# Optimization experiments

Hardware: AMD Instinct MI355X
Metric: run time of the kernel (lower is better)

The kernel has to match this reference:

```python
import jax, jax.numpy as jnp
import numpy as np


def setup_inputs() -> dict:
    key = jax.random.key(0)
    ks = jax.random.split(key, 8)
    B, C, H, W = 4, 256, 64, 64
    Cqk = C // 8
    s = 0.05
    return {
        "x": jax.random.normal(ks[0], (B, C, H, W), jnp.float32),
        "Wq": jax.random.normal(ks[1], (Cqk, C), jnp.float32) * s,
        "bq": jax.random.normal(ks[2], (Cqk,), jnp.float32) * s,
        "Wk": jax.random.normal(ks[3], (Cqk, C), jnp.float32) * s,
        "bk": jax.random.normal(ks[4], (Cqk,), jnp.float32) * s,
        "Wv": jax.random.normal(ks[5], (C, C), jnp.float32) * s,
        "bv": jax.random.normal(ks[6], (C,), jnp.float32) * s,
        "gamma": jax.random.normal(ks[7], (1,), jnp.float32),
    }


def reference(x, Wq, bq, Wk, bk, Wv, bv, gamma):
    B, C, H, W = x.shape
    N = H * W
    xf = x.reshape(B, C, N)                      # [B,C,N]
    # 1x1 convs == channel matmuls
    q = jnp.einsum('oc,bcn->bon', Wq, xf) + bq[None, :, None]   # [B,C/8,N]
    k = jnp.einsum('oc,bcn->bon', Wk, xf) + bk[None, :, None]   # [B,C/8,N]
    v = jnp.einsum('oc,bcn->bon', Wv, xf) + bv[None, :, None]   # [B,C,N]
    # scores[b,i,j] = <q[:,i], k[:,j]>; softmax over j (last dim)
    scores = jnp.einsum('bci,bcj->bij', q, k)                   # [B,N,N]
    attn = jax.nn.softmax(scores, axis=-1)
    # out[b,c,i] = sum_j v[b,c,j] * attn[b,i,j]
    out = jnp.einsum('bcj,bij->bci', v, attn).reshape(B, C, H, W)
    return gamma[0] * out + x
```

## Files before the change

kernel.cpp:

```cpp
#include <hip/hip_runtime.h>


#define B_ 4
#define C_ 256
#define N_ 4096
#define CQK 32

typedef __attribute__((ext_vector_type(8))) short short8;
typedef __attribute__((ext_vector_type(4))) short short4v;
typedef __attribute__((ext_vector_type(16))) float f32x16;
typedef __attribute__((ext_vector_type(4))) float f32x4;

__device__ __forceinline__ unsigned short f2bf(float f) {
  unsigned int u = __builtin_bit_cast(unsigned int, f);
  u = (u + 0x7fffu + ((u >> 16) & 1u)) >> 16;
  return (unsigned short)u;
}
__device__ __forceinline__ float bf2f(unsigned short s) {
  unsigned int u = ((unsigned int)s) << 16;
  return __builtin_bit_cast(float, u);
}
__device__ __forceinline__ f32x16 mfma16(short8 a, short8 b, f32x16 c) {
  return __builtin_amdgcn_mfma_f32_32x32x16_bf16(a, b, c, 0, 0, 0);
}
__device__ __forceinline__ int swz64(int row, int col) {
  return row * 64 + ((((col >> 3) ^ row) & 7) << 3) + (col & 7);
}
__device__ __forceinline__ int swz32(int row, int col) {
  return row * 32 + ((((col >> 3) ^ row) & 3) << 3) + (col & 7);
}

__global__ __launch_bounds__(256) void k_prep(
    const float* __restrict__ x, unsigned short* __restrict__ xthi,
    unsigned short* __restrict__ xtlo,
    const float* __restrict__ Wq, const float* __restrict__ Wk,
    const float* __restrict__ Wv,
    unsigned short* __restrict__ wqh, unsigned short* __restrict__ wql,
    unsigned short* __restrict__ wkh, unsigned short* __restrict__ wkl,
    unsigned short* __restrict__ wvh, unsigned short* __restrict__ wvl) {
  __shared__ __align__(16) float tile[64 * 65];
  const int bi = blockIdx.x;
  const int t = threadIdx.x;
  if (bi < 1024) {
    const int it = bi & 63, ct = (bi >> 6) & 3, b = bi >> 8;
    const int i0 = it * 64, c0 = ct * 64;
    {
      const int i = t & 63, cb = t >> 6;
#pragma unroll
      for (int z = 0; z < 16; ++z) {
        const int c = z * 4 + cb;
        tile[i * 65 + c] = x[(b * C_ + c0 + c) * N_ + i0 + i];
      }
    }
    __syncthreads();
    {
      const int ii = t >> 2, p = t & 3;
      short8 h0, h1, l0, l1;
#pragma unroll
      for (int e = 0; e < 16; ++e) {
        const float f = tile[ii * 65 + p * 16 + e];
        const unsigned short hb = f2bf(f);
        const unsigned short lb = f2bf(f - bf2f(hb));
        if (e < 8) { h0[e] = (short)hb; l0[e] = (short)lb; }
        else       { h1[e - 8] = (short)hb; l1[e - 8] = (short)lb; }
      }
      const int base = (b * N_ + i0 + ii) * C_ + c0 + p * 16;
      *(short8*)(xthi + base) = h0;
      *(short8*)(xthi + base + 8) = h1;
      *(short8*)(xtlo + base) = l0;
      *(short8*)(xtlo + base + 8) = l1;
    }
  } else {
    const int e = (bi - 1024) * 256 + t;
    const float* src; unsigned short *hi, *lo; int idx;
    if (e < 8192)        { src = Wq; hi = wqh; lo = wql; idx = e; }
    else if (e < 16384)  { src = Wk; hi = wkh; lo = wkl; idx = e - 8192; }
    else                 { src = Wv; hi = wvh; lo = wvl; idx = e - 16384; }
    const float f = src[idx];
    const unsigned short h = f2bf(f);
    hi[idx] = h;
    lo[idx] = f2bf(f - bf2f(h));
  }
}

__global__ __launch_bounds__(256) void k_proj(
    const unsigned short* __restrict__ wqh, const unsigned short* __restrict__ wql,
    const unsigned short* __restrict__ wkh, const unsigned short* __restrict__ wkl,
    const unsigned short* __restrict__ wvh, const unsigned short* __restrict__ wvl,
    const unsigned short* __restrict__ xthi, const unsigned short* __restrict__ xtlo,
    const float* __restrict__ bq, const float* __restrict__ bk,
    const float* __restrict__ bv,
    unsigned short* __restrict__ qhg, unsigned short* __restrict__ qlg,
    unsigned short* __restrict__ khg, unsigned short* __restrict__ klg,
    unsigned short* __restrict__ vg) {
  __shared__ __align__(16) char sm[33792];
  unsigned short* awh = (unsigned short*)sm;
  unsigned short* awl = awh + 4096;
  unsigned short* bxh = awl + 4096;
  unsigned short* bxl = bxh + 4096;
  float* qt = (float*)sm;

  const int it = blockIdx.x, ot = blockIdx.y, b = blockIdx.z;
  const int i0 = it * 64, o0 = ot * 64;
  const int t = threadIdx.x, lane = t & 63, w = t >> 6, h = lane >> 5;
  const int mb = w >> 1, nb = w & 1;
  const int srow = t >> 2, sp = t & 3;

  const int og = o0 + srow;
  const unsigned short *wh, *wl;
  if (og < 32)      { wh = wqh + og * C_;        wl = wql + og * C_; }
  else if (og < 64) { wh = wkh + (og - 32) * C_; wl = wkl + (og - 32) * C_; }
  else              { wh = wvh + (og - 64) * C_; wl = wvl + (og - 64) * C_; }
  const unsigned short* xh = xthi + (b * N_ + i0 + srow) * C_;
  const unsigned short* xl = xtlo + (b * N_ + i0 + srow) * C_;

  f32x16 acc;
#pragma unroll
  for (int e = 0; e < 16; ++e) acc[e] = 0.f;
  const int m = 32 * mb + (lane & 31);
  const int n = 32 * nb + (lane & 31);

  for (int kt = 0; kt < 4; ++kt) {
    const int cb = kt * 64 + sp * 16;
    *(short8*)&awh[swz64(srow, sp * 16)]     = *(const short8*)(wh + cb);
    *(short8*)&awh[swz64(srow, sp * 16 + 8)] = *(const short8*)(wh + cb + 8);
    *(short8*)&awl[swz64(srow, sp * 16)]     = *(const short8*)(wl + cb);
    *(short8*)&awl[swz64(srow, sp * 16 + 8)] = *(const short8*)(wl + cb + 8);
    *(short8*)&bxh[swz64(srow, sp * 16)]     = *(const short8*)(xh + cb);
    *(short8*)&bxh[swz64(srow, sp * 16 + 8)] = *(const short8*)(xh + cb + 8);
    *(short8*)&bxl[swz64(srow, sp * 16)]     = *(const short8*)(xl + cb);
    *(short8*)&bxl[swz64(srow, sp * 16 + 8)] = *(const short8*)(xl + cb + 8);
    __syncthreads();
#pragma unroll
    for (int kk = 0; kk < 4; ++kk) {
      const int kb = kk * 16 + h * 8;
      const short8 ah  = *(const short8*)&awh[swz64(m, kb)];
      const short8 al2 = *(const short8*)&awl[swz64(m, kb)];
      const short8 bh  = *(const short8*)&bxh[swz64(n, kb)];
      const short8 bl2 = *(const short8*)&bxl[swz64(n, kb)];
      acc = mfma16(ah, bh, acc);
      acc = mfma16(ah, bl2, acc);
      acc = mfma16(al2, bh, acc);
    }
    __syncthreads();
  }

  if (ot > 0) {
#pragma unroll
    for (int e = 0; e < 16; ++e) {
      const int r = 32 * mb + (e & 3) + 8 * (e >> 2) + 4 * h;
      const int oc = o0 - 64 + r;
      vg[(b * C_ + oc) * N_ + i0 + n] = f2bf(acc[e] + bv[oc]);
    }
  } else {
#pragma unroll
    for (int e = 0; e < 16; ++e) {
      const int r = 32 * mb + (e & 3) + 8 * (e >> 2) + 4 * h;
      const float bias = (r < 32) ? bq[r] : bk[r - 32];
      qt[r * 65 + n] = acc[e] + bias;
    }
    __syncthreads();
    const int ii = t >> 2;
    short8 hv0, hv1, lv0, lv1;
#pragma unroll
    for (int e = 0; e < 16; ++e) {
      const float f = qt[(sp * 16 + e) * 65 + ii];
      const unsigned short hb = f2bf(f);
      const unsigned short lb = f2bf(f - bf2f(hb));
      if (e < 8) { hv0[e] = (short)hb; lv0[e] = (short)lb; }
      else       { hv1[e - 8] = (short)hb; lv1[e - 8] = (short)lb; }
    }
    if (sp < 2) {
      const int base = (b * N_ + i0 + ii) * CQK + sp * 16;
      *(short8*)(qhg + base) = hv0; *(short8*)(qhg + base + 8) = hv1;
      *(short8*)(qlg + base) = lv0; *(short8*)(qlg + base + 8) = lv1;
    } else {
      const int base = (b * N_ + i0 + ii) * CQK + sp * 16 - 32;
      *(short8*)(khg + base) = hv0; *(short8*)(khg + base + 8) = hv1;
      *(short8*)(klg + base) = lv0; *(short8*)(klg + base + 8) = lv1;
    }
  }
}

__global__ __launch_bounds__(512, 4) void k_flash(
    const unsigned short* __restrict__ qhg, const unsigned short* __restrict__ qlg,
    const unsigned short* __restrict__ khg, const unsigned short* __restrict__ klg,
    const unsigned short* __restrict__ vg,
    unsigned short* __restrict__ Opart, float* __restrict__ mlpart) {
  __shared__ __align__(16) char sm[65536];
  unsigned short* kh = (unsigned short*)sm;
  unsigned short* kl = (unsigned short*)(sm + 4096);
  unsigned short* vt = (unsigned short*)(sm + 8192);
  float* stf = (float*)(sm + 40960);
  char* stb = sm + 40960;
  float* alphaf = (float*)(sm + 57344);
  float* otf = (float*)sm;

  const int blk = blockIdx.x;
  const int b = (blk >> 1) & 3;
  const int half = blk & 1;
  const int qt_ = blk >> 3;
  const int q0 = qt_ * 64;
  const int jbase = half * 2048;
  const int t = threadIdx.x, lane = t & 63, w = t >> 6, h = lane >> 5;
  const int l31 = lane & 31;
  const int r_sm = t >> 3, p_sm = t & 7;

  {
    const int r = (t & 255) >> 2, g = t & 3;
    const unsigned short* src = ((t < 256) ? qhg : qlg) + (b * N_ + q0 + r) * CQK + g * 8;
    unsigned short* dst = (t < 256) ? kh : kl;
    *(short8*)&dst[swz32(r, g * 8)] = *(const short8*)src;
  }
  __syncthreads();
  const int mbs = (w >> 1) & 1, nbs = w & 1;
  short8 qfh[2], qfl[2];
  {
    const int mq = 32 * mbs + l31;
#pragma unroll
    for (int kk = 0; kk < 2; ++kk) {
      qfh[kk] = *(const short8*)&kh[swz32(mq, kk * 16 + h * 8)];
      qfl[kk] = *(const short8*)&kl[swz32(mq, kk * 16 + h * 8)];
    }
  }
  __syncthreads();

  f32x16 acc0, acc1;
#pragma unroll
  for (int e = 0; e < 16; ++e) { acc0[e] = 0.f; acc1[e] = 0.f; }
  float m_run = -1e30f, l_run = 0.f;

  for (int kt = 0; kt < 32; ++kt) {
    const int j0 = jbase + kt * 64;
    {
      const int r = (t & 255) >> 2, g = t & 3;
      const unsigned short* src = ((t < 256) ? khg : klg) + (b * N_ + j0 + r) * CQK + g * 8;
      unsigned short* dst = (t < 256) ? kh : kl;
      *(short8*)&dst[swz32(r, g * 8)] = *(const short8*)src;
    }
#pragma unroll
    for (int pass = 0; pass < 4; ++pass) {
      const int gid = pass * 512 + t;
      const int c = gid >> 3, g = gid & 7;
      *(short8*)&vt[swz64(c, g * 8)] =
          *(const short8*)(vg + (b * C_ + c) * N_ + j0 + g * 8);
    }
    __syncthreads();
    if (w < 4) {
      f32x16 sa;
#pragma unroll
      for (int e = 0; e < 16; ++e) sa[e] = 0.f;
      const int jn = 32 * nbs + l31;
#pragma unroll
      for (int kk = 0; kk < 2; ++kk) {
        const short8 bh = *(const short8*)&kh[swz32(jn, kk * 16 + h * 8)];
        const short8 bl = *(const short8*)&kl[swz32(jn, kk * 16 + h * 8)];
        sa = mfma16(qfh[kk], bh, sa);
        sa = mfma16(qfh[kk], bl, sa);
        sa = mfma16(qfl[kk], bh, sa);
      }
#pragma unroll
      for (int e = 0; e < 16; ++e) {
        const int ri = 32 * mbs + (e & 3) + 8 * (e >> 2) + 4 * h;
        stf[ri * 64 + ((((jn >> 2) ^ ri) & 15) << 2) + (jn & 3)] = sa[e];
      }
    }
    __syncthreads();
    {
      float* p0 = stf + r_sm * 64 + ((((2 * p_sm) ^ r_sm) & 15) << 2);
      float* p1 = stf + r_sm * 64 + ((((2 * p_sm + 1) ^ r_sm) & 15) << 2);
      const f32x4 a0 = *(const f32x4*)p0;
      const f32x4 a1 = *(const f32x4*)p1;
      float s[8];
#pragma unroll
      for (int e = 0; e < 4; ++e) { s[e] = a0[e]; s[4 + e] = a1[e]; }
      float mx = s[0];
#pragma unroll
      for (int e = 1; e < 8; ++e) mx = fmaxf(mx, s[e]);
      mx = fmaxf(mx, __shfl_xor(mx, 1));
      mx = fmaxf(mx, __shfl_xor(mx, 2));
      mx = fmaxf(mx, __shfl_xor(mx, 4));
      const float mnew = fmaxf(m_run, mx);
      const float al = __expf(m_run - mnew);
      float ts = 0.f;
      short8 pv8;
#pragma unroll
      for (int e = 0; e < 8; ++e) {
        const float pe = __expf(s[e] - mnew);
        ts += pe;
        pv8[e] = (short)f2bf(pe);
      }
      ts += __shfl_xor(ts, 1);
      ts += __shfl_xor(ts, 2);
      ts += __shfl_xor(ts, 4);
      l_run = l_run * al + ts;
      m_run = mnew;
      *(short8*)p0 = pv8;
      if (p_sm == 0) alphaf[r_sm] = al;
    }
    __syncthreads();
#pragma unroll
    for (int eq = 0; eq < 4; ++eq) {
      const f32x4 av0 = *(const f32x4*)&alphaf[4 * h + 8 * eq];
      const f32x4 av1 = *(const f32x4*)&alphaf[32 + 4 * h + 8 * eq];
#pragma unroll
      for (int q = 0; q < 4; ++q) {
        acc0[4 * eq + q] *= av0[q];
        acc1[4 * eq + q] *= av1[q];
      }
    }
    {
      const int crow = 32 * w + l31;
#pragma unroll
      for (int kk = 0; kk < 4; ++kk) {
        const int g0 = ((4 * kk + 2 * h) ^ l31) & 15;
        const short8 pa0 = *(const short8*)(stb + l31 * 256 + (g0 << 4));
        const short8 pa1 = *(const short8*)(stb + (32 + l31) * 256 + (g0 << 4));
        const short8 vf = *(const short8*)&vt[swz64(crow, kk * 16 + h * 8)];
        acc0 = mfma16(pa0, vf, acc0);
        acc1 = mfma16(pa1, vf, acc1);
      }
    }
    __syncthreads();
  }

  if (p_sm == 0) {
    mlpart[blk * 128 + r_sm] = m_run;
    mlpart[blk * 128 + 64 + r_sm] = l_run;
  }
  {
    const int cc = 32 * w + l31;
#pragma unroll
    for (int e = 0; e < 16; ++e) {
      const int r0 = (e & 3) + 8 * (e >> 2) + 4 * h;
      otf[cc * 64 + ((((r0 >> 2) ^ cc) & 15) << 2) + (r0 & 3)] = acc0[e];
      const int r1 = 32 + r0;
      otf[cc * 64 + ((((r1 >> 2) ^ cc) & 15) << 2) + (r1 & 3)] = acc1[e];
    }
  }
  __syncthreads();
#pragma unroll
  for (int pass = 0; pass < 8; ++pass) {
    const int idx = pass * 512 + t;
    const int c = idx >> 4, gi = idx & 15;
    const f32x4 ov = *(const f32x4*)(otf + c * 64 + (((gi ^ c) & 15) << 2));
    short4v hv;
#pragma unroll
    for (int q = 0; q < 4; ++q) {
      const _Float16 hf = (_Float16)ov[q];
      hv[q] = __builtin_bit_cast(short, hf);
    }
    *(short4v*)(Opart + blk * 16384 + c * 64 + gi * 4) = hv;
  }
}

__global__ __launch_bounds__(256) void k_combine(
    const unsigned short* __restrict__ Opart, const float* __restrict__ mlpart,
    const float* __restrict__ x, const float* __restrict__ gamma,
    float* __restrict__ out) {
  const int cb = blockIdx.x;
  const int b = cb & 3, qt_ = cb >> 2;
  const int q0 = qt_ * 64;
  const int blk1 = (qt_ << 3) | (b << 1);
  const int blk2 = blk1 | 1;
  const int t = threadIdx.x;
  const int i = t & 63, cg = t >> 6;

  const float m1 = mlpart[blk1 * 128 + i], l1 = mlpart[blk1 * 128 + 64 + i];
  const float m2 = mlpart[blk2 * 128 + i], l2 = mlpart[blk2 * 128 + 64 + i];
  const float M = fmaxf(m1, m2);
  const float w1 = __expf(m1 - M), w2 = __expf(m2 - M);
  const float inv = 1.f / (w1 * l1 + w2 * l2);
  const float gm = gamma[0];
  const float s1 = gm * w1 * inv, s2 = gm * w2 * inv;

  const unsigned short* p1 = Opart + blk1 * 16384 + i;
  const unsigned short* p2 = Opart + blk2 * 16384 + i;
#pragma unroll 4
  for (int c = cg; c < C_; c += 4) {
    const float o1 = (float)__builtin_bit_cast(_Float16, p1[c * 64]);
    const float o2 = (float)__builtin_bit_cast(_Float16, p2[c * 64]);
    const int g = (b * C_ + c) * N_ + q0 + i;
    out[g] = s1 * o1 + s2 * o2 + x[g];
  }
}

extern "C" void kernel_launch(void* const* d_in, const int* in_sizes, int n_in,
                              void* d_out, int out_size, void* d_ws, size_t ws_size,
                              hipStream_t stream) {
  const float* x     = (const float*)d_in[0];
  const float* Wq    = (const float*)d_in[1];
  const float* bq    = (const float*)d_in[2];
  const float* Wk    = (const float*)d_in[3];
  const float* bk    = (const float*)d_in[4];
  const float* Wv    = (const float*)d_in[5];
  const float* bv    = (const float*)d_in[6];
  const float* gamma = (const float*)d_in[7];
  float* out = (float*)d_out;
  (void)in_sizes; (void)n_in; (void)out_size; (void)ws_size;

  char* ws = (char*)d_ws;
  size_t off = 0;
  auto carve = [&](size_t bytes) -> char* {
    char* p = ws + off;
    off += (bytes + 255) & ~(size_t)255;
    return p;
  };
  unsigned short* xthi = (unsigned short*)carve((size_t)B_ * N_ * C_ * 2);
  unsigned short* xtlo = (unsigned short*)carve((size_t)B_ * N_ * C_ * 2);
  unsigned short* wqh  = (unsigned short*)carve(32 * 256 * 2);
  unsigned short* wql  = (unsigned short*)carve(32 * 256 * 2);
  unsigned short* wkh  = (unsigned short*)carve(32 * 256 * 2);
  unsigned short* wkl  = (unsigned short*)carve(32 * 256 * 2);
  unsigned short* wvh  = (unsigned short*)carve(256 * 256 * 2);
  unsigned short* wvl  = (unsigned short*)carve(256 * 256 * 2);
  unsigned short* qhg  = (unsigned short*)carve((size_t)B_ * N_ * CQK * 2);
  unsigned short* qlg  = (unsigned short*)carve((size_t)B_ * N_ * CQK * 2);
  unsigned short* khg  = (unsigned short*)carve((size_t)B_ * N_ * CQK * 2);
  unsigned short* klg  = (unsigned short*)carve((size_t)B_ * N_ * CQK * 2);
  unsigned short* vg   = (unsigned short*)carve((size_t)B_ * C_ * N_ * 2);
  unsigned short* Opart = (unsigned short*)carve((size_t)512 * 16384 * 2);
  float* mlpart = (float*)carve((size_t)512 * 128 * 4);

  k_prep<<<1344, 256, 0, stream>>>(x, xthi, xtlo, Wq, Wk, Wv,
                                   wqh, wql, wkh, wkl, wvh, wvl);
  k_proj<<<dim3(64, 5, B_), 256, 0, stream>>>(wqh, wql, wkh, wkl, wvh, wvl,
                                              xthi, xtlo, bq, bk, bv,
                                              qhg, qlg, khg, klg, vg);
  k_flash<<<512, 512, 0, stream>>>(qhg, qlg, khg, klg, vg, Opart, mlpart);
  k_combine<<<256, 256, 0, stream>>>(Opart, mlpart, x, gamma, out);
}
```

Before: 213.9 us.

## Prefetch K and V through registers, drop K LDS staging and barriers

K fragments for the QK^T MFMAs now load straight from global into registers, one tile ahead, so K is no longer staged in shared memory. The next V tile is register-prefetched two tiles ahead and written only to the LDS rows owned by the same wave, which removes a full block barrier per iteration. Some barriers become raw s_barrier with explicit lgkmcnt waits, and setprio raises wave priority around the MFMA sections. The trade-off is higher register pressure and reliance on per-wave ownership of V rows for correctness without a sync.

```diff
diff --git a/kernel.cpp b/kernel.cpp
--- a/kernel.cpp
+++ b/kernel.cpp
@@ -26,9 +26,13 @@
 __device__ __forceinline__ int swz64(int row, int col) {
   return row * 64 + ((((col >> 3) ^ row) & 7) << 3) + (col & 7);
 }
-__device__ __forceinline__ int swz32(int row, int col) {
-  return row * 32 + ((((col >> 3) ^ row) & 3) << 3) + (col & 7);
-}
+
+#define BAR_SYNC                                        \
+  do {                                                  \
+    asm volatile("s_waitcnt lgkmcnt(0)" ::: "memory");  \
+    __builtin_amdgcn_s_barrier();                       \
+  } while (0)
+#define BAR_FAST __builtin_amdgcn_s_barrier()
 
 __global__ __launch_bounds__(256) void k_prep(
     const float* __restrict__ x, unsigned short* __restrict__ xthi,
@@ -188,12 +192,10 @@
     const unsigned short* __restrict__ vg,
     unsigned short* __restrict__ Opart, float* __restrict__ mlpart) {
   __shared__ __align__(16) char sm[65536];
-  unsigned short* kh = (unsigned short*)sm;
-  unsigned short* kl = (unsigned short*)(sm + 4096);
-  unsigned short* vt = (unsigned short*)(sm + 8192);
-  float* stf = (float*)(sm + 40960);
-  char* stb = sm + 40960;
-  float* alphaf = (float*)(sm + 57344);
+  float* stf = (float*)sm;
+  char* stb = sm;
+  unsigned short* vt = (unsigned short*)(sm + 16384);
+  float* alphaf = (float*)(sm + 49152);
   float* otf = (float*)sm;
 
   const int blk = blockIdx.x;
@@ -205,25 +207,42 @@
   const int t = threadIdx.x, lane = t & 63, w = t >> 6, h = lane >> 5;
   const int l31 = lane & 31;
   const int r_sm = t >> 3, p_sm = t & 7;
-
-  {
-    const int r = (t & 255) >> 2, g = t & 3;
-    const unsigned short* src = ((t < 256) ? qhg : qlg) + (b * N_ + q0 + r) * CQK + g * 8;
-    unsigned short* dst = (t < 256) ? kh : kl;
-    *(short8*)&dst[swz32(r, g * 8)] = *(const short8*)src;
-  }
-  __syncthreads();
   const int mbs = (w >> 1) & 1, nbs = w & 1;
-  short8 qfh[2], qfl[2];
-  {
-    const int mq = 32 * mbs + l31;
+
+  const int vrow = 32 * w + (lane >> 3);
+  const int vcol = (lane & 7) * 8;
+  const unsigned short* vsrc =
+      vg + (size_t)(b * C_ + vrow) * N_ + jbase + vcol;
+
+  short8 vst[4];
+#pragma unroll
+  for (int p = 0; p < 4; ++p)
+    vst[p] = *(const short8*)(vsrc + p * 8 * N_);
+
+  short8 qfh[2], qfl[2], kfh[2], kfl[2];
+  const unsigned short* qph =
+      qhg + (size_t)(b * N_ + q0 + 32 * mbs + l31) * CQK + h * 8;
+  const unsigned short* qpl =
+      qlg + (size_t)(b * N_ + q0 + 32 * mbs + l31) * CQK + h * 8;
+  const unsigned short* kph =
+      khg + (size_t)(b * N_ + jbase + 32 * nbs + l31) * CQK + h * 8;
+  const unsigned short* kpl =
+      klg + (size_t)(b * N_ + jbase + 32 * nbs + l31) * CQK + h * 8;
+  if (w < 4) {
 #pragma unroll
     for (int kk = 0; kk < 2; ++kk) {
-      qfh[kk] = *(const short8*)&kh[swz32(mq, kk * 16 + h * 8)];
-      qfl[kk] = *(const short8*)&kl[swz32(mq, kk * 16 + h * 8)];
-    }
-  }
-  __syncthreads();
+      qfh[kk] = *(const short8*)(qph + kk * 16);
+      qfl[kk] = *(const short8*)(qpl + kk * 16);
+      kfh[kk] = *(const short8*)(kph + kk * 16);
+      kfl[kk] = *(const short8*)(kpl + kk * 16);
+    }
+  }
+#pragma unroll
+  for (int p = 0; p < 4; ++p)
+    *(short8*)&vt[swz64(vrow + 8 * p, vcol)] = vst[p];
+#pragma unroll
+  for (int p = 0; p < 4; ++p)
+    vst[p] = *(const short8*)(vsrc + 64 + p * 8 * N_);
 
   f32x16 acc0, acc1;
 #pragma unroll
@@ -231,41 +250,33 @@
   float m_run = -1e30f, l_run = 0.f;
 
   for (int kt = 0; kt < 32; ++kt) {
-    const int j0 = jbase + kt * 64;
-    {
-      const int r = (t & 255) >> 2, g = t & 3;
-      const unsigned short* src = ((t < 256) ? khg : klg) + (b * N_ + j0 + r) * CQK + g * 8;
-      unsigned short* dst = (t < 256) ? kh : kl;
-      *(short8*)&dst[swz32(r, g * 8)] = *(const short8*)src;
-    }
-#pragma unroll
-    for (int pass = 0; pass < 4; ++pass) {
-      const int gid = pass * 512 + t;
-      const int c = gid >> 3, g = gid & 7;
-      *(short8*)&vt[swz64(c, g * 8)] =
-          *(const short8*)(vg + (b * C_ + c) * N_ + j0 + g * 8);
-    }
-    __syncthreads();
+    BAR_FAST;
     if (w < 4) {
       f32x16 sa;
 #pragma unroll
       for (int e = 0; e < 16; ++e) sa[e] = 0.f;
+      __builtin_amdgcn_s_setprio(1);
+#pragma unroll
+      for (int kk = 0; kk < 2; ++kk) {
+        sa = mfma16(qfh[kk], kfh[kk], sa);
+        sa = mfma16(qfh[kk], kfl[kk], sa);
+        sa = mfma16(qfl[kk], kfh[kk], sa);
+      }
+      __builtin_amdgcn_s_setprio(0);
       const int jn = 32 * nbs + l31;
-#pragma unroll
-      for (int kk = 0; kk < 2; ++kk) {
-        const short8 bh = *(const short8*)&kh[swz32(jn, kk * 16 + h * 8)];
-        const short8 bl = *(const short8*)&kl[swz32(jn, kk * 16 + h * 8)];
-        sa = mfma16(qfh[kk], bh, sa);
-        sa = mfma16(qfh[kk], bl, sa);
-        sa = mfma16(qfl[kk], bh, sa);
-      }
 #pragma unroll
       for (int e = 0; e < 16; ++e) {
         const int ri = 32 * mbs + (e & 3) + 8 * (e >> 2) + 4 * h;
         stf[ri * 64 + ((((jn >> 2) ^ ri) & 15) << 2) + (jn & 3)] = sa[e];
       }
-    }
-    __syncthreads();
+      const int ko = ((kt + 1 < 32) ? (kt + 1) : 31) * 64 * CQK;
+#pragma unroll
+      for (int kk = 0; kk < 2; ++kk) {
+        kfh[kk] = *(const short8*)(kph + ko + kk * 16);
+        kfl[kk] = *(const short8*)(kpl + ko + kk * 16);
+      }
+    }
+    BAR_SYNC;
     {
       float* p0 = stf + r_sm * 64 + ((((2 * p_sm) ^ r_sm) & 15) << 2);
       float* p1 = stf + r_sm * 64 + ((((2 * p_sm + 1) ^ r_sm) & 15) << 2);
@@ -298,7 +309,7 @@
       *(short8*)p0 = pv8;
       if (p_sm == 0) alphaf[r_sm] = al;
     }
-    __syncthreads();
+    BAR_SYNC;
 #pragma unroll
     for (int eq = 0; eq < 4; ++eq) {
       const f32x4 av0 = *(const f32x4*)&alphaf[4 * h + 8 * eq];
@@ -311,6 +322,7 @@
     }
     {
       const int crow = 32 * w + l31;
+      __builtin_amdgcn_s_setprio(1);
 #pragma unroll
       for (int kk = 0; kk < 4; ++kk) {
         const int g0 = ((4 * kk + 2 * h) ^ l31) & 15;
@@ -320,14 +332,22 @@
         acc0 = mfma16(pa0, vf, acc0);
         acc1 = mfma16(pa1, vf, acc1);
       }
-    }
-    __syncthreads();
+      __builtin_amdgcn_s_setprio(0);
+    }
+#pragma unroll
+    for (int p = 0; p < 4; ++p)
+      *(short8*)&vt[swz64(vrow + 8 * p, vcol)] = vst[p];
+    const int vo = ((kt + 2 < 32) ? (kt + 2) : 31) * 64;
+#pragma unroll
+    for (int p = 0; p < 4; ++p)
+      vst[p] = *(const short8*)(vsrc + vo + p * 8 * N_);
   }
 
   if (p_sm == 0) {
     mlpart[blk * 128 + r_sm] = m_run;
     mlpart[blk * 128 + 64 + r_sm] = l_run;
   }
+  BAR_FAST;
   {
     const int cc = 32 * w + l31;
 #pragma unroll
@@ -338,7 +358,7 @@
       otf[cc * 64 + ((((r1 >> 2) ^ cc) & 15) << 2) + (r1 & 3)] = acc1[e];
     }
   }
-  __syncthreads();
+  BAR_SYNC;
 #pragma unroll
   for (int pass = 0; pass < 8; ++pass) {
     const int idx = pass * 512 + t;
```

Result: slower. 243.6 us (+13.9%).

## Prefetch K/V tiles via direct global-to-LDS loads overlapped with compute

Applied to the files above, without the earlier changes.

Replaces the per-iteration register-staged K and V tile loads in the flash kernel with global_load_lds async copies. The next K tile is issued after the score stage and the next V tile after the PV MFMAs, and they are synchronised with explicit s_waitcnt vmcnt counters and raw barriers instead of __syncthreads. The Q fragments are now loaded straight from global memory into registers, the LDS regions are rearranged so the score buffer no longer overlaps K/V, and s_setprio is raised around the MFMA blocks. The goal is to hide global latency behind compute. The cost is fragile manual counter-based synchronisation, and there is a risk of races if the vmcnt accounting is wrong.

```diff
diff --git a/kernel.cpp b/kernel.cpp
--- a/kernel.cpp
+++ b/kernel.cpp
@@ -29,6 +29,18 @@
 __device__ __forceinline__ int swz32(int row, int col) {
   return row * 32 + ((((col >> 3) ^ row) & 3) << 3) + (col & 7);
 }
+
+#define GL16(gp, lp)                                                     \
+  __builtin_amdgcn_global_load_lds(                                      \
+      (const __attribute__((address_space(1))) unsigned int*)(gp),       \
+      (__attribute__((address_space(3))) unsigned int*)(lp), 16, 0, 0)
+
+#define WAITCNT(s) asm volatile("s_waitcnt " s ::: "memory")
+#define BARRIER()                         \
+  do {                                    \
+    __builtin_amdgcn_s_barrier();         \
+    asm volatile("" ::: "memory");        \
+  } while (0)
 
 __global__ __launch_bounds__(256) void k_prep(
     const float* __restrict__ x, unsigned short* __restrict__ xthi,
@@ -188,11 +200,11 @@
     const unsigned short* __restrict__ vg,
     unsigned short* __restrict__ Opart, float* __restrict__ mlpart) {
   __shared__ __align__(16) char sm[65536];
-  unsigned short* kh = (unsigned short*)sm;
-  unsigned short* kl = (unsigned short*)(sm + 4096);
-  unsigned short* vt = (unsigned short*)(sm + 8192);
-  float* stf = (float*)(sm + 40960);
-  char* stb = sm + 40960;
+  float* stf = (float*)sm;
+  char* stb = sm;
+  unsigned short* kh = (unsigned short*)(sm + 16384);
+  unsigned short* kl = (unsigned short*)(sm + 20480);
+  unsigned short* vt = (unsigned short*)(sm + 24576);
   float* alphaf = (float*)(sm + 57344);
   float* otf = (float*)sm;
 
@@ -205,25 +217,38 @@
   const int t = threadIdx.x, lane = t & 63, w = t >> 6, h = lane >> 5;
   const int l31 = lane & 31;
   const int r_sm = t >> 3, p_sm = t & 7;
-
-  {
-    const int r = (t & 255) >> 2, g = t & 3;
-    const unsigned short* src = ((t < 256) ? qhg : qlg) + (b * N_ + q0 + r) * CQK + g * 8;
-    unsigned short* dst = (t < 256) ? kh : kl;
-    *(short8*)&dst[swz32(r, g * 8)] = *(const short8*)src;
-  }
-  __syncthreads();
   const int mbs = (w >> 1) & 1, nbs = w & 1;
+
+  const int krow = 16 * (w & 3) + (lane >> 2);
+  const int kg = (lane & 3) ^ (krow & 3);
+  const unsigned short* kgsrc = ((w < 4) ? khg : klg) +
+      (size_t)(b * N_ + jbase + krow) * CQK + kg * 8;
+  unsigned short* kldst = ((w < 4) ? kh : kl) + (w & 3) * 512;
+  const int vc = 32 * w + (lane >> 3);
+  const int vgg = (lane & 7) ^ ((lane >> 3) & 7);
+  const unsigned short* vgsrc =
+      vg + (size_t)(b * C_ + vc) * N_ + jbase + vgg * 8;
+  unsigned short* vldst = vt + 32 * w * 64;
+
+  GL16(kgsrc, kldst);
+#pragma unroll
+  for (int q = 0; q < 4; ++q)
+    GL16(vgsrc + q * 8 * N_, vldst + q * 8 * 64);
+
   short8 qfh[2], qfl[2];
   {
-    const int mq = 32 * mbs + l31;
-#pragma unroll
-    for (int kk = 0; kk < 2; ++kk) {
-      qfh[kk] = *(const short8*)&kh[swz32(mq, kk * 16 + h * 8)];
-      qfl[kk] = *(const short8*)&kl[swz32(mq, kk * 16 + h * 8)];
-    }
-  }
-  __syncthreads();
+    const unsigned short* qph =
+        qhg + (size_t)(b * N_ + q0 + 32 * mbs + l31) * CQK + h * 8;
+    const unsigned short* qpl =
+        qlg + (size_t)(b * N_ + q0 + 32 * mbs + l31) * CQK + h * 8;
+    if (w < 4) {
+#pragma unroll
+      for (int kk = 0; kk < 2; ++kk) {
+        qfh[kk] = *(const short8*)(qph + kk * 16);
+        qfl[kk] = *(const short8*)(qpl + kk * 16);
+      }
+    }
+  }
 
   f32x16 acc0, acc1;
 #pragma unroll
@@ -231,26 +256,14 @@
   float m_run = -1e30f, l_run = 0.f;
 
   for (int kt = 0; kt < 32; ++kt) {
-    const int j0 = jbase + kt * 64;
-    {
-      const int r = (t & 255) >> 2, g = t & 3;
-      const unsigned short* src = ((t < 256) ? khg : klg) + (b * N_ + j0 + r) * CQK + g * 8;
-      unsigned short* dst = (t < 256) ? kh : kl;
-      *(short8*)&dst[swz32(r, g * 8)] = *(const short8*)src;
-    }
-#pragma unroll
-    for (int pass = 0; pass < 4; ++pass) {
-      const int gid = pass * 512 + t;
-      const int c = gid >> 3, g = gid & 7;
-      *(short8*)&vt[swz64(c, g * 8)] =
-          *(const short8*)(vg + (b * C_ + c) * N_ + j0 + g * 8);
-    }
-    __syncthreads();
+    WAITCNT("vmcnt(4) lgkmcnt(0)");
+    BARRIER();
     if (w < 4) {
       f32x16 sa;
 #pragma unroll
       for (int e = 0; e < 16; ++e) sa[e] = 0.f;
       const int jn = 32 * nbs + l31;
+      __builtin_amdgcn_s_setprio(1);
 #pragma unroll
       for (int kk = 0; kk < 2; ++kk) {
         const short8 bh = *(const short8*)&kh[swz32(jn, kk * 16 + h * 8)];
@@ -259,13 +272,19 @@
         sa = mfma16(qfh[kk], bl, sa);
         sa = mfma16(qfl[kk], bh, sa);
       }
+      __builtin_amdgcn_s_setprio(0);
 #pragma unroll
       for (int e = 0; e < 16; ++e) {
         const int ri = 32 * mbs + (e & 3) + 8 * (e >> 2) + 4 * h;
         stf[ri * 64 + ((((jn >> 2) ^ ri) & 15) << 2) + (jn & 3)] = sa[e];
       }
     }
-    __syncthreads();
+    WAITCNT("lgkmcnt(0)");
+    BARRIER();
+    {
+      const int ktn = (kt + 1 < 32) ? kt + 1 : 31;
+      GL16(kgsrc + ktn * 64 * CQK, kldst);
+    }
     {
       float* p0 = stf + r_sm * 64 + ((((2 * p_sm) ^ r_sm) & 15) << 2);
       float* p1 = stf + r_sm * 64 + ((((2 * p_sm + 1) ^ r_sm) & 15) << 2);
@@ -298,7 +317,8 @@
       *(short8*)p0 = pv8;
       if (p_sm == 0) alphaf[r_sm] = al;
     }
-    __syncthreads();
+    WAITCNT("lgkmcnt(0)");
+    BARRIER();
 #pragma unroll
     for (int eq = 0; eq < 4; ++eq) {
       const f32x4 av0 = *(const f32x4*)&alphaf[4 * h + 8 * eq];
@@ -309,8 +329,10 @@
         acc1[4 * eq + q] *= av1[q];
       }
     }
+    WAITCNT("vmcnt(1)");
     {
       const int crow = 32 * w + l31;
+      __builtin_amdgcn_s_setprio(1);
 #pragma unroll
       for (int kk = 0; kk < 4; ++kk) {
         const int g0 = ((4 * kk + 2 * h) ^ l31) & 15;
@@ -320,14 +342,24 @@
         acc0 = mfma16(pa0, vf, acc0);
         acc1 = mfma16(pa1, vf, acc1);
       }
-    }
-    __syncthreads();
+      __builtin_amdgcn_s_setprio(0);
+    }
+    WAITCNT("lgkmcnt(0)");
+    {
+      const int ktv = (kt + 1 < 32) ? kt + 1 : 31;
+      const unsigned short* vs = vgsrc + ktv * 64;
+#pragma unroll
+      for (int q = 0; q < 4; ++q)
+        GL16(vs + q * 8 * N_, vldst + q * 8 * 64);
+    }
   }
 
   if (p_sm == 0) {
     mlpart[blk * 128 + r_sm] = m_run;
     mlpart[blk * 128 + 64 + r_sm] = l_run;
   }
+  WAITCNT("vmcnt(0) lgkmcnt(0)");
+  BARRIER();
   {
     const int cc = 32 * w + l31;
 #pragma unroll
@@ -338,7 +370,8 @@
       otf[cc * 64 + ((((r1 >> 2) ^ cc) & 15) << 2) + (r1 & 3)] = acc1[e];
     }
   }
-  __syncthreads();
+  WAITCNT("lgkmcnt(0)");
+  BARRIER();
 #pragma unroll
   for (int pass = 0; pass < 8; ++pass) {
     const int idx = pass * 512 + t;
```

New measurement: 200.2 us. 6.4% less time.
